# Optimization experiments

Hardware: AMD Instinct MI355X
Metric: run time of the kernel (lower is better)

Reference implementation:

```python
import jax, jax.numpy as jnp
from jax import lax
import numpy as np

GRID_SIZE = 3
SPLINE_ORDER = 2
N_BASIS = GRID_SIZE + SPLINE_ORDER  # 5
_H = 2.0 / GRID_SIZE  # grid_range [-1, 1]
# extended uniform grid, shape (1, grid_size + 2*spline_order + 1) = (1, 8)
GRID = (jnp.arange(-SPLINE_ORDER, GRID_SIZE + SPLINE_ORDER + 1, dtype=jnp.float32) * _H - 1.0)[None, :]


def b_splines(x):
    """Cox-de Boor B-spline bases. x: (..., F) -> (..., F, N_BASIS)."""
    x = x[..., None]
    g = GRID
    bases = ((x >= g[:, :-1]) & (x < g[:, 1:])).astype(x.dtype)
    for p in range(1, SPLINE_ORDER + 1):
        left = (x - g[:, :-(p + 1)]) / (g[:, p:-1] - g[:, :-(p + 1)])
        right = (g[:, p + 1:] - x) / (g[:, p + 1:] - g[:, 1:-p])
        bases = left * bases[..., :-1] + right * bases[..., 1:]
    return bases


def kan_conv(x, base_w, spline_w, scaler):
    """Unfold-based KAN conv: x NCHW -> NCHW. base_w (O,F), spline_w (O,F,K), scaler (O,F)."""
    # patches: (B, C*kh*kw, H', W'), channel-major feature ordering like torch unfold
    p = lax.conv_general_dilated_patches(x, (4, 4), (2, 2), ((1, 1), (1, 1)))
    f = jnp.transpose(p, (0, 2, 3, 1))  # (B, H', W', F)
    base = jax.nn.relu(f) @ base_w.T
    spl = jnp.einsum('bhwfk,ofk->bhwo', b_splines(f), spline_w * scaler[..., None])
    return jnp.transpose(base + spl, (0, 3, 1, 2))


def batchnorm(x, gamma, beta):
    # train-mode BN over (B,H,W) per channel, eps=1e-5 (torch default)
    m = x.mean((0, 2, 3), keepdims=True)
    v = x.var((0, 2, 3), keepdims=True)
    return (x - m) * lax.rsqrt(v + 1e-5) * gamma[None, :, None, None] + beta[None, :, None, None]


def setup_inputs() -> dict:
    key = jax.random.key(0)
    ks = jax.random.split(key, 32)
    B = 512
    chans = [(3, 32), (32, 64), (64, 128), (128, 128)]
    inp = {"x": jax.random.normal(ks[0], (B, 3, 32, 32), jnp.float32)}
    i = 1
    for li, (cin, cout) in enumerate(chans, start=1):
        F = cin * 16
        inp[f"bw{li}"] = jax.random.normal(ks[i], (cout, F), jnp.float32) * (0.8 / np.sqrt(F)); i += 1
        inp[f"sw{li}"] = jax.random.normal(ks[i], (cout, F, N_BASIS), jnp.float32) * (0.8 / np.sqrt(F)); i += 1
        inp[f"sc{li}"] = jnp.ones((cout, F), jnp.float32) + 0.05 * jax.random.normal(ks[i], (cout, F), jnp.float32); i += 1
    for bi, c in [(1, 64), (2, 128), (3, 128)]:
        inp[f"g{bi}"] = jnp.ones((c,), jnp.float32)
        inp[f"b{bi}"] = jnp.zeros((c,), jnp.float32)
    inp["fc_w"] = jax.random.normal(ks[i], (1, 128), jnp.float32) * (1.0 / np.sqrt(128)); i += 1
    inp["fc_b"] = jnp.zeros((1,), jnp.float32)
    return inp


def reference(x, bw1, sw1, sc1, bw2, sw2, sc2, bw3, sw3, sc3, bw4, sw4, sc4,
              g1, b1, g2, b2, g3, b3, fc_w, fc_b):
    h = kan_conv(x, bw1, sw1, sc1)                     # (B,32,16,16)
    h = kan_conv(h, bw2, sw2, sc2)                     # (B,64,8,8)
    h = batchnorm(h, g1, b1)
    h = kan_conv(h, bw3, sw3, sc3)                     # (B,128,4,4)
    h = batchnorm(h, g2, b2)
    h = kan_conv(h, bw4, sw4, sc4)                     # (B,128,2,2)
    h = batchnorm(h, g3, b3)
    h = h.mean((2, 3))                                 # AdaptiveAvgPool2d(1) + Flatten -> (B,128)
    return jax.nn.sigmoid(h @ fc_w.T + fc_b)           # (B,1)
```

## Files before the change

kernel.cpp:

```cpp
#include <hip/hip_runtime.h>
#include <hip/hip_bf16.h>
#include <math.h>

#define DEVINL __device__ __forceinline__

typedef short short8 __attribute__((ext_vector_type(8)));
typedef float f32x4 __attribute__((ext_vector_type(4)));

DEVINL unsigned short f2bf(float f) {
    union { float f; unsigned int u; } c; c.f = f;
    unsigned int u = c.u;
    return (unsigned short)((u + 0x7fffu + ((u >> 16) & 1u)) >> 16);
}

DEVINL unsigned int packbf2(float a, float b) {
    union { __hip_bfloat162 h; unsigned int u; } c;
    c.h = __float22bfloat162_rn(make_float2(a, b));
    return c.u;
}

DEVINL void gload_lds16(const unsigned int* g, unsigned int* l) {
    __builtin_amdgcn_global_load_lds((const __attribute__((address_space(1))) unsigned int*)g,
                                     (__attribute__((address_space(3))) unsigned int*)l, 16, 0, 0);
}

DEVINL uint4 expand_frag(float v) {
    float relu = fmaxf(v, 0.f);
    float u = fmaf(v, 1.5f, 3.5f);
    float fj = floorf(u);
    int j = (int)fj;
    float t = u - fj;
    float omt = 1.f - t;
    float v2 = 0.5f * omt * omt;
    float v1 = fmaf(t, omt, 0.5f);
    float v0 = 0.5f * t * t;
    float b[5];
#pragma unroll
    for (int i = 0; i < 5; ++i)
        b[i] = (i == j) ? v0 : (i == j - 1) ? v1 : (i == j - 2) ? v2 : 0.f;
    uint4 r;
    r.x = packbf2(relu, b[0]);
    r.y = packbf2(b[1], b[2]);
    r.z = packbf2(b[3], b[4]);
    r.w = 0u;
    return r;
}

template <int CIN, int COUT>
__global__ __launch_bounds__(256) void prep_wfrag(const float* __restrict__ bw,
                                                  const float* __restrict__ sw,
                                                  const float* __restrict__ sc,
                                                  unsigned short* __restrict__ wf) {
    constexpr int F = CIN * 16;
    constexpr int NT = COUT / 16;
    int idx = blockIdx.x * 256 + threadIdx.x;
    if (idx >= CIN * COUT * 128) return;
    int j = idx & 7;
    int lane = (idx >> 3) & 63;
    int t = idx >> 9;
    int ks = t & 3;
    int t2 = t >> 2;
    int nt = t2 % NT;
    int c = t2 / NT;
    int k = ks * 32 + ((lane >> 4) << 3) + j;
    int tap = k >> 3, s = k & 7;
    int f = c * 16 + tap;
    int o = nt * 16 + (lane & 15);
    float v = 0.f;
    if (s == 0) v = bw[o * F + f];
    else if (s <= 5) v = sw[(o * F + f) * 5 + (s - 1)] * sc[o * F + f];
    wf[idx] = f2bf(v);
}

template <int CIN, int COUT, int HOUT, int WOUT, int WM, int WN, int MT, int CPS,
          int UB, bool HASBN, bool SPLITOUT, int RPAD>
__global__ __launch_bounds__(256) void kan_conv_fused(
    const float* __restrict__ in, const unsigned short* __restrict__ wf,
    const float* __restrict__ bnscale, const float* __restrict__ bnshift,
    float* __restrict__ out) {
    constexpr int HIN = HOUT * 2, WIN = WOUT * 2, W2 = WOUT;
    constexpr int NT = COUT / 16;
    constexpr int NTW = NT / WN;
    constexpr int BM = WM * MT * 16;
    constexpr int IMG_POS = HOUT * WOUT;
    constexpr int NIMG = BM / IMG_POS;
    constexpr int RS = WIN + RPAD;
    constexpr int IMG_STRIDE = HIN * RS + 1;
    constexpr int ASLOTS = NIMG * IMG_STRIDE + 1;
    constexpr int M_TOT = 512 * IMG_POS;
    constexpr int EV = NIMG * HIN * WIN;
    constexpr int EITER = (EV + 255) / 256;
    static_assert(WM * WN == 4, "4 waves");
    static_assert(CPS % UB == 0, "UB divides CPS");

    __shared__ uint4 A_e[UB][ASLOTS];
    __shared__ uint4 B_l[UB][COUT * 16];

    const int tid = threadIdx.x;
    const int lane = tid & 63;
    const int w = tid >> 6;
    const int wm = w % WM;
    const int wn = w / WM;
    const int g = lane >> 4;
    const int r16 = lane & 15;
    const int m0 = blockIdx.x * BM;
    const int b0 = m0 / IMG_POS;
    const int c0 = SPLITOUT ? blockIdx.y * CPS : 0;

    int aoff[MT];
    int vmask = 0;
#pragma unroll
    for (int mt = 0; mt < MT; ++mt) {
        int p = (wm * MT + mt) * 16 + r16;
        int m = m0 + p;
        int ow = m % WOUT;
        int oh = (m / WOUT) % HOUT;
        int bl = p / IMG_POS;
        int iw = 2 * ow - 1 + g;
        bool iv = (iw >= 0) && (iw < WIN);
        aoff[mt] = 1 + bl * IMG_STRIDE + (2 * oh) * RS + (iw & 1) * W2 + (iw >> 1);
#pragma unroll
        for (int ks = 0; ks < 4; ++ks) {
            bool vv = iv && !(oh == 0 && ks == 0) && !(oh == HOUT - 1 && ks == 3);
            vmask |= (vv ? 1 : 0) << (mt * 4 + ks);
        }
    }

    if (tid < UB) A_e[tid][0] = expand_frag(0.f);

    f32x4 acc[MT][NTW];
#pragma unroll
    for (int mt = 0; mt < MT; ++mt)
#pragma unroll
        for (int n = 0; n < NTW; ++n) acc[mt][n] = f32x4{0.f, 0.f, 0.f, 0.f};

    for (int cc = 0; cc < CPS; cc += UB) {
#pragma unroll
        for (int u = 0; u < UB; ++u) {
            const int ch = c0 + cc + u;
            const unsigned int* bsrc = (const unsigned int*)(wf + (size_t)ch * (COUT * 128));
            unsigned int* bdst = (unsigned int*)&B_l[u][0];
#pragma unroll
            for (int r2 = 0; r2 < NT; ++r2)
                gload_lds16(bsrc + ((r2 << 8) + tid) * 4, bdst + ((r2 << 8) + tid) * 4);
        }
#pragma unroll
        for (int u = 0; u < UB; ++u) {
            const int ch = c0 + cc + u;
            float bsc = 1.f, bsh = 0.f;
            if (HASBN) { bsc = bnscale[ch]; bsh = bnshift[ch]; }
#pragma unroll
            for (int ii = 0; ii < EITER; ++ii) {
                int e = tid + ii * 256;
                if (e < EV) {
                    int bl = e / (HIN * WIN);
                    int r = e - bl * (HIN * WIN);
                    int ih = r / WIN;
                    int iw = r - ih * WIN;
                    float v = in[(((size_t)(b0 + bl) * CIN + ch) * HIN + ih) * WIN + iw];
                    if (HASBN) v = fmaf(v, bsc, bsh);
                    A_e[u][1 + bl * IMG_STRIDE + ih * RS + (iw & 1) * W2 + (iw >> 1)] = expand_frag(v);
                }
            }
        }
        __syncthreads();
#pragma unroll
        for (int u = 0; u < UB; ++u) {
#pragma unroll
            for (int ks = 0; ks < 4; ++ks) {
                short8 bf[NTW];
#pragma unroll
                for (int n = 0; n < NTW; ++n)
                    bf[n] = *(const short8*)&B_l[u][(((wn * NTW + n) * 4 + ks) << 6) + lane];
#pragma unroll
                for (int mt = 0; mt < MT; ++mt) {
                    int slot = ((vmask >> (mt * 4 + ks)) & 1) ? (aoff[mt] + (ks - 1) * RS) : 0;
                    short8 af = *(const short8*)&A_e[u][slot];
#pragma unroll
                    for (int n = 0; n < NTW; ++n)
                        acc[mt][n] = __builtin_amdgcn_mfma_f32_16x16x32_bf16(af, bf[n], acc[mt][n], 0, 0, 0);
                }
            }
        }
        __syncthreads();
    }

    const int colo = lane & 15;
    const int row4 = (lane >> 4) * 4;
#pragma unroll
    for (int mt = 0; mt < MT; ++mt) {
#pragma unroll
        for (int n = 0; n < NTW; ++n) {
            int o = (wn * NTW + n) * 16 + colo;
#pragma unroll
            for (int rr = 0; rr < 4; ++rr) {
                int p = (wm * MT + mt) * 16 + row4 + rr;
                int m = m0 + p;
                if (SPLITOUT) {
                    out[((size_t)blockIdx.y * M_TOT + m) * COUT + o] = acc[mt][n][rr];
                } else {
                    int ow = m % WOUT;
                    int t = m / WOUT;
                    int oh = t % HOUT;
                    int b = t / HOUT;
                    out[((b * COUT + o) * HOUT + oh) * WOUT + ow] = acc[mt][n][rr];
                }
            }
        }
    }
}

template <int NS, int COUT, int HOUT, int WOUT>
__global__ __launch_bounds__(256) void reduce_split(const float* __restrict__ P,
                                                    float* __restrict__ out) {
    constexpr int M = 512 * HOUT * WOUT;
    int idx4 = blockIdx.x * 256 + threadIdx.x;
    if (idx4 >= M * COUT / 4) return;
    f32x4 s = {0.f, 0.f, 0.f, 0.f};
#pragma unroll
    for (int i = 0; i < NS; ++i) {
        f32x4 v = *(const f32x4*)&P[(size_t)i * M * COUT + idx4 * 4];
        s += v;
    }
    int o0 = (idx4 * 4) % COUT;
    int m = (idx4 * 4) / COUT;
    int ow = m % WOUT;
    int t = m / WOUT;
    int oh = t % HOUT;
    int b = t / HOUT;
#pragma unroll
    for (int q = 0; q < 4; ++q)
        out[((b * COUT + o0 + q) * HOUT + oh) * WOUT + ow] = s[q];
}

template <int C, int HW, int S>
__global__ __launch_bounds__(256) void bn_partial(const float* __restrict__ a,
                                                  float* __restrict__ part) {
    constexpr int BS = 512 / S;
    constexpr int NE = BS * HW;
    int c = blockIdx.x / S, s = blockIdx.x % S;
    int tid = threadIdx.x;
    float sm = 0.f, s2 = 0.f;
    for (int e = tid; e < NE; e += 256) {
        int b = s * BS + e / HW;
        int hw = e % HW;
        float v = a[((size_t)b * C + c) * HW + hw];
        sm += v;
        s2 += v * v;
    }
    __shared__ float r0[256], r1[256];
    r0[tid] = sm; r1[tid] = s2;
    __syncthreads();
    for (int off = 128; off > 0; off >>= 1) {
        if (tid < off) { r0[tid] += r0[tid + off]; r1[tid] += r1[tid + off]; }
        __syncthreads();
    }
    if (tid == 0) {
        part[(c * S + s) * 2] = r0[0];
        part[(c * S + s) * 2 + 1] = r1[0];
    }
}

template <int C, int HW, int S>
__global__ void bn_finish(const float* __restrict__ part, const float* __restrict__ gamma,
                          const float* __restrict__ beta, float* __restrict__ scale,
                          float* __restrict__ shift) {
    int c = threadIdx.x;
    if (c >= C) return;
    float sm = 0.f, s2 = 0.f;
#pragma unroll 4
    for (int s = 0; s < S; ++s) {
        sm += part[(c * S + s) * 2];
        s2 += part[(c * S + s) * 2 + 1];
    }
    const float invN = 1.f / (float)(512 * HW);
    float mean = sm * invN;
    float var = s2 * invN - mean * mean;
    float rs = rsqrtf(var + 1e-5f);
    float scl = gamma[c] * rs;
    scale[c] = scl;
    shift[c] = beta[c] - mean * scl;
}

__global__ void head_ker(const float* __restrict__ a4, const float* __restrict__ scale,
                         const float* __restrict__ shift, const float* __restrict__ fcw,
                         const float* __restrict__ fcb, float* __restrict__ out) {
    int b = blockIdx.x;
    int lane = threadIdx.x;
    float acc = 0.0f;
#pragma unroll
    for (int j = 0; j < 2; ++j) {
        int o = lane + 64 * j;
        const float* p = a4 + (b * 128 + o) * 4;
        float sv = p[0] + p[1] + p[2] + p[3];
        float pooled = fmaf(sv * 0.25f, scale[o], shift[o]);
        acc = fmaf(pooled, fcw[o], acc);
    }
#pragma unroll
    for (int off = 32; off > 0; off >>= 1) acc += __shfl_down(acc, off);
    if (lane == 0) out[b] = 1.0f / (1.0f + expf(-(acc + fcb[0])));
}

extern "C" void kernel_launch(void* const* d_in, const int* in_sizes, int n_in,
                              void* d_out, int out_size, void* d_ws, size_t ws_size,
                              hipStream_t stream) {
    const float* x   = (const float*)d_in[0];
    const float* bw1 = (const float*)d_in[1];
    const float* sw1 = (const float*)d_in[2];
    const float* sc1 = (const float*)d_in[3];
    const float* bw2 = (const float*)d_in[4];
    const float* sw2 = (const float*)d_in[5];
    const float* sc2 = (const float*)d_in[6];
    const float* bw3 = (const float*)d_in[7];
    const float* sw3 = (const float*)d_in[8];
    const float* sc3 = (const float*)d_in[9];
    const float* bw4 = (const float*)d_in[10];
    const float* sw4 = (const float*)d_in[11];
    const float* sc4 = (const float*)d_in[12];
    const float* g1  = (const float*)d_in[13];
    const float* b1  = (const float*)d_in[14];
    const float* g2  = (const float*)d_in[15];
    const float* b2  = (const float*)d_in[16];
    const float* g3  = (const float*)d_in[17];
    const float* b3  = (const float*)d_in[18];
    const float* fcw = (const float*)d_in[19];
    const float* fcb = (const float*)d_in[20];

    float* ws = (float*)d_ws;
    float* a1 = ws;
    float* a2 = a1 + 4194304;
    float* a3 = a2 + 2097152;
    float* a4 = a3 + 1048576;
    float* bnsc1 = a4 + 262144;
    float* bnsh1 = bnsc1 + 64;
    float* bnsc2 = bnsh1 + 64;
    float* bnsh2 = bnsc2 + 128;
    float* bnsc3 = bnsh2 + 128;
    float* bnsh3 = bnsc3 + 128;
    unsigned short* wf1 = (unsigned short*)(bnsh3 + 128);
    unsigned short* wf2 = wf1 + 12288;
    unsigned short* wf3 = wf2 + 262144;
    unsigned short* wf4 = wf3 + 1048576;
    float* part1 = (float*)(wf4 + 2097152);
    float* part2 = part1 + 2048;
    float* part3 = part2 + 4096;
    float* P3 = a1;
    float* P4 = a2;

    prep_wfrag<3, 32><<<48, 256, 0, stream>>>(bw1, sw1, sc1, wf1);
    prep_wfrag<32, 64><<<1024, 256, 0, stream>>>(bw2, sw2, sc2, wf2);
    prep_wfrag<64, 128><<<4096, 256, 0, stream>>>(bw3, sw3, sc3, wf3);
    prep_wfrag<128, 128><<<8192, 256, 0, stream>>>(bw4, sw4, sc4, wf4);

    kan_conv_fused<3, 32, 16, 16, 4, 1, 4, 3, 3, false, false, 0>
        <<<512, 256, 0, stream>>>(x, wf1, nullptr, nullptr, a1);
    kan_conv_fused<32, 64, 8, 8, 2, 2, 2, 32, 2, false, false, 0>
        <<<512, 256, 0, stream>>>(a1, wf2, nullptr, nullptr, a2);
    bn_partial<64, 64, 16><<<1024, 256, 0, stream>>>(a2, part1);
    bn_finish<64, 64, 16><<<1, 64, 0, stream>>>(part1, g1, b1, bnsc1, bnsh1);
    kan_conv_fused<64, 128, 4, 4, 1, 4, 4, 16, 2, true, true, 1>
        <<<dim3(128, 4), 256, 0, stream>>>(a2, wf3, bnsc1, bnsh1, P3);
    reduce_split<4, 128, 4, 4><<<1024, 256, 0, stream>>>(P3, a3);
    bn_partial<128, 16, 16><<<2048, 256, 0, stream>>>(a3, part2);
    bn_finish<128, 16, 16><<<1, 128, 0, stream>>>(part2, g2, b2, bnsc2, bnsh2);
    kan_conv_fused<128, 128, 2, 2, 1, 4, 2, 16, 2, true, true, 0>
        <<<dim3(64, 8), 256, 0, stream>>>(a3, wf4, bnsc2, bnsh2, P4);
    reduce_split<8, 128, 2, 2><<<256, 256, 0, stream>>>(P4, a4);
    bn_partial<128, 4, 8><<<1024, 256, 0, stream>>>(a4, part3);
    bn_finish<128, 4, 8><<<1, 128, 0, stream>>>(part3, g3, b3, bnsc3, bnsh3);
    head_ker<<<512, 64, 0, stream>>>(a4, bnsc3, bnsh3, fcw, fcb, (float*)d_out);
}
```

Before: 146.7 us.

## Double-buffer conv channel staging, split output channels, fold BN finish and prep launches

```diff
diff --git a/kernel.cpp b/kernel.cpp
--- a/kernel.cpp
+++ b/kernel.cpp
@@ -46,22 +46,16 @@
     return r;
 }
 
-template <int CIN, int COUT>
-__global__ __launch_bounds__(256) void prep_wfrag(const float* __restrict__ bw,
-                                                  const float* __restrict__ sw,
-                                                  const float* __restrict__ sc,
-                                                  unsigned short* __restrict__ wf) {
-    constexpr int F = CIN * 16;
-    constexpr int NT = COUT / 16;
-    int idx = blockIdx.x * 256 + threadIdx.x;
-    if (idx >= CIN * COUT * 128) return;
+DEVINL void prep_one(int idx, int F, int NTT, const float* __restrict__ bw,
+                     const float* __restrict__ sw, const float* __restrict__ sc,
+                     unsigned short* __restrict__ wf) {
     int j = idx & 7;
     int lane = (idx >> 3) & 63;
     int t = idx >> 9;
     int ks = t & 3;
     int t2 = t >> 2;
-    int nt = t2 % NT;
-    int c = t2 / NT;
+    int nt = t2 % NTT;
+    int c = t2 / NTT;
     int k = ks * 32 + ((lane >> 4) << 3) + j;
     int tap = k >> 3, s = k & 7;
     int f = c * 16 + tap;
@@ -72,13 +66,33 @@
     wf[idx] = f2bf(v);
 }
 
-template <int CIN, int COUT, int HOUT, int WOUT, int WM, int WN, int MT, int CPS,
-          int UB, bool HASBN, bool SPLITOUT, int RPAD>
-__global__ __launch_bounds__(256) void kan_conv_fused(
+__global__ __launch_bounds__(256) void prep_all(
+    const float* __restrict__ bw1, const float* __restrict__ sw1, const float* __restrict__ sc1,
+    const float* __restrict__ bw2, const float* __restrict__ sw2, const float* __restrict__ sc2,
+    const float* __restrict__ bw3, const float* __restrict__ sw3, const float* __restrict__ sc3,
+    const float* __restrict__ bw4, const float* __restrict__ sw4, const float* __restrict__ sc4,
+    unsigned short* __restrict__ wf1, unsigned short* __restrict__ wf2,
+    unsigned short* __restrict__ wf3, unsigned short* __restrict__ wf4) {
+    int idx = blockIdx.x * 256 + threadIdx.x;
+    const int N1 = 3 * 32 * 128;
+    const int N2 = 32 * 64 * 128;
+    const int N3 = 64 * 128 * 128;
+    const int N4 = 128 * 128 * 128;
+    if (idx < N1) prep_one(idx, 48, 2, bw1, sw1, sc1, wf1);
+    else if (idx < N1 + N2) prep_one(idx - N1, 512, 4, bw2, sw2, sc2, wf2);
+    else if (idx < N1 + N2 + N3) prep_one(idx - N1 - N2, 1024, 8, bw3, sw3, sc3, wf3);
+    else if (idx < N1 + N2 + N3 + N4) prep_one(idx - N1 - N2 - N3, 2048, 8, bw4, sw4, sc4, wf4);
+}
+
+template <int CIN, int COUTT, int NSP, int HOUT, int WOUT, int WM, int WN, int MT,
+          int CPS, bool HASBN, int BNS, int NBN, bool SPLITOUT, int RPAD>
+__global__ __launch_bounds__(256) void kan_conv_pipe(
     const float* __restrict__ in, const unsigned short* __restrict__ wf,
-    const float* __restrict__ bnscale, const float* __restrict__ bnshift,
-    float* __restrict__ out) {
+    const float* __restrict__ part, const float* __restrict__ gamma,
+    const float* __restrict__ beta, float* __restrict__ out) {
     constexpr int HIN = HOUT * 2, WIN = WOUT * 2, W2 = WOUT;
+    constexpr int COUT = COUTT / NSP;
+    constexpr int NTT = COUTT / 16;
     constexpr int NT = COUT / 16;
     constexpr int NTW = NT / WN;
     constexpr int BM = WM * MT * 16;
@@ -91,10 +105,9 @@
     constexpr int EV = NIMG * HIN * WIN;
     constexpr int EITER = (EV + 255) / 256;
     static_assert(WM * WN == 4, "4 waves");
-    static_assert(CPS % UB == 0, "UB divides CPS");
-
-    __shared__ uint4 A_e[UB][ASLOTS];
-    __shared__ uint4 B_l[UB][COUT * 16];
+
+    __shared__ uint4 A_e[2][ASLOTS];
+    __shared__ uint4 B_l[2][NT * 256];
 
     const int tid = threadIdx.x;
     const int lane = tid & 63;
@@ -105,7 +118,9 @@
     const int r16 = lane & 15;
     const int m0 = blockIdx.x * BM;
     const int b0 = m0 / IMG_POS;
-    const int c0 = SPLITOUT ? blockIdx.y * CPS : 0;
+    const int nh = (NSP > 1) ? ((int)blockIdx.y % NSP) : 0;
+    const int kslice = (NSP > 1) ? ((int)blockIdx.y / NSP) : (SPLITOUT ? (int)blockIdx.y : 0);
+    const int c0 = SPLITOUT ? kslice * CPS : 0;
 
     int aoff[MT];
     int vmask = 0;
@@ -126,7 +141,7 @@
         }
     }
 
-    if (tid < UB) A_e[tid][0] = expand_frag(0.f);
+    if (tid < 2) A_e[tid][0] = expand_frag(0.f);
 
     f32x4 acc[MT][NTW];
 #pragma unroll
@@ -134,55 +149,76 @@
 #pragma unroll
         for (int n = 0; n < NTW; ++n) acc[mt][n] = f32x4{0.f, 0.f, 0.f, 0.f};
 
-    for (int cc = 0; cc < CPS; cc += UB) {
-#pragma unroll
-        for (int u = 0; u < UB; ++u) {
-            const int ch = c0 + cc + u;
-            const unsigned int* bsrc = (const unsigned int*)(wf + (size_t)ch * (COUT * 128));
-            unsigned int* bdst = (unsigned int*)&B_l[u][0];
-#pragma unroll
-            for (int r2 = 0; r2 < NT; ++r2)
-                gload_lds16(bsrc + ((r2 << 8) + tid) * 4, bdst + ((r2 << 8) + tid) * 4);
-        }
-#pragma unroll
-        for (int u = 0; u < UB; ++u) {
-            const int ch = c0 + cc + u;
-            float bsc = 1.f, bsh = 0.f;
-            if (HASBN) { bsc = bnscale[ch]; bsh = bnshift[ch]; }
-#pragma unroll
-            for (int ii = 0; ii < EITER; ++ii) {
-                int e = tid + ii * 256;
-                if (e < EV) {
-                    int bl = e / (HIN * WIN);
-                    int r = e - bl * (HIN * WIN);
-                    int ih = r / WIN;
-                    int iw = r - ih * WIN;
-                    float v = in[(((size_t)(b0 + bl) * CIN + ch) * HIN + ih) * WIN + iw];
-                    if (HASBN) v = fmaf(v, bsc, bsh);
-                    A_e[u][1 + bl * IMG_STRIDE + ih * RS + (iw & 1) * W2 + (iw >> 1)] = expand_frag(v);
-                }
+    auto STAGE = [&](int cc, int buf) {
+        const int ch = c0 + cc;
+        const unsigned int* bsrc = (const unsigned int*)wf + ((size_t)ch * NTT + nh * NT) * 1024;
+        unsigned int* bdst = (unsigned int*)&B_l[buf][0];
+#pragma unroll
+        for (int r2 = 0; r2 < NT; ++r2)
+            gload_lds16(bsrc + r2 * 1024 + tid * 4, bdst + r2 * 1024 + tid * 4);
+    };
+
+    auto EXPAND = [&](int cc, int buf) {
+        const int ch = c0 + cc;
+        float bsc = 1.f, bsh = 0.f;
+        if (HASBN) {
+            float sm = 0.f, s2 = 0.f;
+#pragma unroll 4
+            for (int s = 0; s < BNS; ++s) {
+                sm += part[(ch * BNS + s) * 2];
+                s2 += part[(ch * BNS + s) * 2 + 1];
             }
-        }
-        __syncthreads();
-#pragma unroll
-        for (int u = 0; u < UB; ++u) {
-#pragma unroll
-            for (int ks = 0; ks < 4; ++ks) {
-                short8 bf[NTW];
+            const float invN = 1.f / (float)NBN;
+            float mean = sm * invN;
+            float var = s2 * invN - mean * mean;
+            float rs = rsqrtf(var + 1e-5f);
+            bsc = gamma[ch] * rs;
+            bsh = beta[ch] - mean * bsc;
+        }
+#pragma unroll
+        for (int ii = 0; ii < EITER; ++ii) {
+            int e = tid + ii * 256;
+            if ((EV % 256 == 0) || e < EV) {
+                int bl = e / (HIN * WIN);
+                int r = e - bl * (HIN * WIN);
+                int ih = r / WIN;
+                int iw = r - ih * WIN;
+                float v = in[(((size_t)(b0 + bl) * CIN + ch) * HIN + ih) * WIN + iw];
+                if (HASBN) v = fmaf(v, bsc, bsh);
+                A_e[buf][1 + bl * IMG_STRIDE + ih * RS + (iw & 1) * W2 + (iw >> 1)] = expand_frag(v);
+            }
+        }
+    };
+
+    auto DOMFMA = [&](int buf) {
+#pragma unroll
+        for (int ks = 0; ks < 4; ++ks) {
+            short8 bf[NTW];
+#pragma unroll
+            for (int n = 0; n < NTW; ++n)
+                bf[n] = *(const short8*)&B_l[buf][(((wn * NTW + n) * 4 + ks) << 6) + lane];
+#pragma unroll
+            for (int mt = 0; mt < MT; ++mt) {
+                int slot = ((vmask >> (mt * 4 + ks)) & 1) ? (aoff[mt] + (ks - 1) * RS) : 0;
+                short8 af = *(const short8*)&A_e[buf][slot];
 #pragma unroll
                 for (int n = 0; n < NTW; ++n)
-                    bf[n] = *(const short8*)&B_l[u][(((wn * NTW + n) * 4 + ks) << 6) + lane];
-#pragma unroll
-                for (int mt = 0; mt < MT; ++mt) {
-                    int slot = ((vmask >> (mt * 4 + ks)) & 1) ? (aoff[mt] + (ks - 1) * RS) : 0;
-                    short8 af = *(const short8*)&A_e[u][slot];
-#pragma unroll
-                    for (int n = 0; n < NTW; ++n)
-                        acc[mt][n] = __builtin_amdgcn_mfma_f32_16x16x32_bf16(af, bf[n], acc[mt][n], 0, 0, 0);
-                }
+                    acc[mt][n] = __builtin_amdgcn_mfma_f32_16x16x32_bf16(af, bf[n], acc[mt][n], 0, 0, 0);
             }
         }
-        __syncthreads();
+    };
+
+    STAGE(0, 0);
+    EXPAND(0, 0);
+    __syncthreads();
+    for (int cc = 0; cc < CPS; ++cc) {
+        int buf = cc & 1;
+        if (cc + 1 < CPS) {
+            STAGE(cc + 1, buf ^ 1);
+            EXPAND(cc + 1, buf ^ 1);
+        }
+        DOMFMA(buf);
+        if (cc + 1 < CPS) __syncthreads();
     }
 
     const int colo = lane & 15;
@@ -191,19 +227,19 @@
     for (int mt = 0; mt < MT; ++mt) {
 #pragma unroll
         for (int n = 0; n < NTW; ++n) {
-            int o = (wn * NTW + n) * 16 + colo;
+            int o = nh * COUT + (wn * NTW + n) * 16 + colo;
 #pragma unroll
             for (int rr = 0; rr < 4; ++rr) {
                 int p = (wm * MT + mt) * 16 + row4 + rr;
                 int m = m0 + p;
                 if (SPLITOUT) {
-                    out[((size_t)blockIdx.y * M_TOT + m) * COUT + o] = acc[mt][n][rr];
+                    out[((size_t)kslice * M_TOT + m) * COUTT + o] = acc[mt][n][rr];
                 } else {
                     int ow = m % WOUT;
                     int t = m / WOUT;
                     int oh = t % HOUT;
                     int b = t / HOUT;
-                    out[((b * COUT + o) * HOUT + oh) * WOUT + ow] = acc[mt][n][rr];
+                    out[((b * COUTT + o) * HOUT + oh) * WOUT + ow] = acc[mt][n][rr];
                 }
             }
         }
@@ -261,39 +297,30 @@
     }
 }
 
-template <int C, int HW, int S>
-__global__ void bn_finish(const float* __restrict__ part, const float* __restrict__ gamma,
-                          const float* __restrict__ beta, float* __restrict__ scale,
-                          float* __restrict__ shift) {
-    int c = threadIdx.x;
-    if (c >= C) return;
-    float sm = 0.f, s2 = 0.f;
-#pragma unroll 4
-    for (int s = 0; s < S; ++s) {
-        sm += part[(c * S + s) * 2];
-        s2 += part[(c * S + s) * 2 + 1];
-    }
-    const float invN = 1.f / (float)(512 * HW);
-    float mean = sm * invN;
-    float var = s2 * invN - mean * mean;
-    float rs = rsqrtf(var + 1e-5f);
-    float scl = gamma[c] * rs;
-    scale[c] = scl;
-    shift[c] = beta[c] - mean * scl;
-}
-
-__global__ void head_ker(const float* __restrict__ a4, const float* __restrict__ scale,
-                         const float* __restrict__ shift, const float* __restrict__ fcw,
-                         const float* __restrict__ fcb, float* __restrict__ out) {
+__global__ void head_ker(const float* __restrict__ a4, const float* __restrict__ part3,
+                         const float* __restrict__ g3, const float* __restrict__ b3,
+                         const float* __restrict__ fcw, const float* __restrict__ fcb,
+                         float* __restrict__ out) {
     int b = blockIdx.x;
     int lane = threadIdx.x;
     float acc = 0.0f;
 #pragma unroll
     for (int j = 0; j < 2; ++j) {
         int o = lane + 64 * j;
+        float sm = 0.f, s2 = 0.f;
+#pragma unroll
+        for (int s = 0; s < 8; ++s) {
+            sm += part3[(o * 8 + s) * 2];
+            s2 += part3[(o * 8 + s) * 2 + 1];
+        }
+        float mean = sm * (1.f / 2048.f);
+        float var = s2 * (1.f / 2048.f) - mean * mean;
+        float rs = rsqrtf(var + 1e-5f);
+        float scl = g3[o] * rs;
+        float sh = b3[o] - mean * scl;
         const float* p = a4 + (b * 128 + o) * 4;
         float sv = p[0] + p[1] + p[2] + p[3];
-        float pooled = fmaf(sv * 0.25f, scale[o], shift[o]);
+        float pooled = fmaf(sv * 0.25f, scl, sh);
         acc = fmaf(pooled, fcw[o], acc);
     }
 #pragma unroll
@@ -331,13 +358,7 @@
     float* a2 = a1 + 4194304;
     float* a3 = a2 + 2097152;
     float* a4 = a3 + 1048576;
-    float* bnsc1 = a4 + 262144;
-    float* bnsh1 = bnsc1 + 64;
-    float* bnsc2 = bnsh1 + 64;
-    float* bnsh2 = bnsc2 + 128;
-    float* bnsc3 = bnsh2 + 128;
-    float* bnsh3 = bnsc3 + 128;
-    unsigned short* wf1 = (unsigned short*)(bnsh3 + 128);
+    unsigned short* wf1 = (unsigned short*)(a4 + 262144);
     unsigned short* wf2 = wf1 + 12288;
     unsigned short* wf3 = wf2 + 262144;
     unsigned short* wf4 = wf3 + 1048576;
@@ -347,26 +368,22 @@
     float* P3 = a1;
     float* P4 = a2;
 
-    prep_wfrag<3, 32><<<48, 256, 0, stream>>>(bw1, sw1, sc1, wf1);
-    prep_wfrag<32, 64><<<1024, 256, 0, stream>>>(bw2, sw2, sc2, wf2);
-    prep_wfrag<64, 128><<<4096, 256, 0, stream>>>(bw3, sw3, sc3, wf3);
-    prep_wfrag<128, 128><<<8192, 256, 0, stream>>>(bw4, sw4, sc4, wf4);
-
-    kan_conv_fused<3, 32, 16, 16, 4, 1, 4, 3, 3, false, false, 0>
-        <<<512, 256, 0, stream>>>(x, wf1, nullptr, nullptr, a1);
-    kan_conv_fused<32, 64, 8, 8, 2, 2, 2, 32, 2, false, false, 0>
-        <<<512, 256, 0, stream>>>(a1, wf2, nullptr, nullptr, a2);
+    prep_all<<<13360, 256, 0, stream>>>(bw1, sw1, sc1, bw2, sw2, sc2,
+                                        bw3, sw3, sc3, bw4, sw4, sc4,
+                                        wf1, wf2, wf3, wf4);
+
+    kan_conv_pipe<3, 32, 1, 16, 16, 4, 1, 4, 3, false, 1, 1, false, 0>
+        <<<512, 256, 0, stream>>>(x, wf1, nullptr, nullptr, nullptr, a1);
+    kan_conv_pipe<32, 64, 2, 8, 8, 2, 2, 2, 32, false, 1, 1, false, 0>
+        <<<dim3(512, 2), 256, 0, stream>>>(a1, wf2, nullptr, nullptr, nullptr, a2);
     bn_partial<64, 64, 16><<<1024, 256, 0, stream>>>(a2, part1);
-    bn_finish<64, 64, 16><<<1, 64, 0, stream>>>(part1, g1, b1, bnsc1, bnsh1);
-    kan_conv_fused<64, 128, 4, 4, 1, 4, 4, 16, 2, true, true, 1>
-        <<<dim3(128, 4), 256, 0, stream>>>(a2, wf3, bnsc1, bnsh1, P3);
+    kan_conv_pipe<64, 128, 2, 4, 4, 1, 4, 4, 16, true, 16, 32768, true, 1>
+        <<<dim3(128, 8), 256, 0, stream>>>(a2, wf3, part1, g1, b1, P3);
     reduce_split<4, 128, 4, 4><<<1024, 256, 0, stream>>>(P3, a3);
     bn_partial<128, 16, 16><<<2048, 256, 0, stream>>>(a3, part2);
-    bn_finish<128, 16, 16><<<1, 128, 0, stream>>>(part2, g2, b2, bnsc2, bnsh2);
-    kan_conv_fused<128, 128, 2, 2, 1, 4, 2, 16, 2, true, true, 0>
-        <<<dim3(64, 8), 256, 0, stream>>>(a3, wf4, bnsc2, bnsh2, P4);
+    kan_conv_pipe<128, 128, 2, 2, 2, 1, 4, 2, 16, true, 16, 8192, true, 0>
+        <<<dim3(64, 16), 256, 0, stream>>>(a3, wf4, part2, g2, b2, P4);
     reduce_split<8, 128, 2, 2><<<256, 256, 0, stream>>>(P4, a4);
     bn_partial<128, 4, 8><<<1024, 256, 0, stream>>>(a4, part3);
-    bn_finish<128, 4, 8><<<1, 128, 0, stream>>>(part3, g3, b3, bnsc3, bnsh3);
-    head_ker<<<512, 64, 0, stream>>>(a4, bnsc3, bnsh3, fcw, fcb, (float*)d_out);
-}
+    head_ker<<<512, 64, 0, stream>>>(a4, part3, g3, b3, fcw, fcb, (float*)d_out);
+}
```

After: 170.7 us. 1.16x slower.
